# Kernel optimization log

Measured on AMD Instinct MI355X. Metric: run time of the kernel, lower is better.

## Reference

```python
import jax, jax.numpy as jnp
import numpy as np
from jax import lax

CLS_TOKEN_ID = 1


def _group_cumsum(x, reset_mask):
    # x: [B, S, D] float, reset_mask: [B, S] bool
    # Running sum that resets at the most recent position where reset_mask is True.
    s = jnp.cumsum(x, axis=1)                      # [B,S,D]
    prime = s - x                                  # exclusive cumsum [B,S,D]
    seq = jnp.arange(x.shape[1])                   # [S]
    idx = seq[None, :] * reset_mask.astype(jnp.int32)   # [B,S]
    idx = lax.cummax(idx, axis=1)[..., None]       # [B,S,1] index of last reset
    return s - jnp.take_along_axis(prime, idx, axis=1)


def group_cummean_weighted(embeddings, reset_mask):
    x = embeddings.astype(jnp.float32)
    ones = jnp.ones(reset_mask.shape + (1,), dtype=jnp.float32)  # [B,S,1]
    scale = _group_cumsum(ones, reset_mask)        # position-in-group count [B,S,1]
    out = _group_cumsum(x * scale, reset_mask) / scale
    return out.astype(embeddings.dtype)


def setup_inputs() -> dict:
    key = jax.random.key(0)
    k1, k2 = jax.random.split(key)
    B, S, D = 8, 4096, 1024
    embeddings = jax.random.normal(k1, (B, S, D), dtype=jnp.float32)
    input_ids = jax.random.randint(k2, (B, S), 0, 64, dtype=jnp.int64)
    return {"embeddings": embeddings, "input_ids": input_ids, "return_final": 0}


def reference(embeddings, input_ids, return_final):
    reset_mask = input_ids == CLS_TOKEN_ID         # [B,S] bool
    out = group_cummean_weighted(embeddings, reset_mask)
    if return_final:
        seq = jnp.arange(input_ids.shape[1])
        end_idx = jnp.max(jnp.where(reset_mask, seq, -1), axis=-1)  # [B]
        return out[jnp.arange(input_ids.shape[0]), end_idx]
    return out
```

## Files before the change

kernel.cpp:

```cpp
#include <hip/hip_runtime.h>


#define B_   8
#define S_   4096
#define D_   1024
#define CL   128
#define NCH  (S_/CL)
#define ROWS (B_*D_)

__global__ __launch_bounds__(256) void k0_count(const int* __restrict__ ids,
                                                float* __restrict__ cntf,
                                                float* __restrict__ invf) {
    int b = blockIdx.x;
    int t = threadIdx.x;
    const int PER = S_ / 256;
    __shared__ int lastr[256];

    int base = t * PER;
    const int* p = ids + b * S_ + base;
    int loc = -1;
#pragma unroll
    for (int j = 0; j < PER; j++)
        if (p[j] == 1) loc = base + j;
    lastr[t] = loc;
    __syncthreads();

    int g = 0;
    for (int i = 0; i < t; i++) {
        int v = lastr[i];
        g = v > g ? v : g;
    }
    for (int j = 0; j < PER; j++) {
        int s = base + j;
        if (p[j] == 1) g = s;
        float c = (float)(s - g + 1);
        cntf[b * S_ + s] = c;
        invf[b * S_ + s] = 1.0f / c;
    }
}

__global__ __launch_bounds__(256) void k1_partial(const float* __restrict__ X,
                                                  const float* __restrict__ cntf,
                                                  float* __restrict__ alpha,
                                                  float* __restrict__ gamma) {
    int blk = blockIdx.x;
    int dt  = blk & 3;
    int k   = (blk >> 2) & (NCH - 1);
    int b   = blk >> 7;
    int t   = threadIdx.x;

    __shared__ float cL[CL];
    if (t < CL) cL[t] = cntf[b * S_ + k * CL + t];
    __syncthreads();

    int d = dt * 256 + t;
    const float* p = X + (size_t)(b * S_ + k * CL) * D_ + d;

    float a = 0.f, g = 0.f;
#pragma unroll 8
    for (int j = 0; j < CL; j++) {
        float x  = p[(size_t)j * D_];
        float cf = cL[j];
        float wl = (float)(j + 1);
        float w  = cf < wl ? cf : wl;
        bool  rst = (cf == 1.0f);
        bool  pre = (cf > wl);
        a = fmaf(x, w, rst ? 0.f : a);
        g = rst ? 0.f : (pre ? g + x : g);
    }
    int row = b * D_ + d;
    alpha[k * ROWS + row] = a;
    gamma[k * ROWS + row] = g;
}

__global__ __launch_bounds__(256) void k2_scan(const float* __restrict__ alpha,
                                               const float* __restrict__ gamma,
                                               const float* __restrict__ cntf,
                                               float* __restrict__ Win) {
    int row = blockIdx.x * 256 + threadIdx.x;
    int b   = row >> 10;
    float W = 0.f, cin = 0.f;
    for (int k = 0; k < NCH; k++) {
        Win[k * ROWS + row] = W;
        float cend = cntf[b * S_ + (k + 1) * CL - 1];
        float a = alpha[k * ROWS + row];
        float g = gamma[k * ROWS + row];
        bool  has = (cend <= (float)CL);
        W   = has ? a : (a + W + g * cin);
        cin = cend;
    }
}

__global__ __launch_bounds__(256) void k3_out(const float* __restrict__ X,
                                              const float* __restrict__ cntf,
                                              const float* __restrict__ invf,
                                              const float* __restrict__ Win,
                                              float* __restrict__ out) {
    int blk = blockIdx.x;
    int dt  = blk & 3;
    int k   = (blk >> 2) & (NCH - 1);
    int b   = blk >> 7;
    int t   = threadIdx.x;

    __shared__ float cL[CL], iL[CL];
    if (t < CL) {
        cL[t] = cntf[b * S_ + k * CL + t];
        iL[t] = invf[b * S_ + k * CL + t];
    }
    __syncthreads();

    int d = dt * 256 + t;
    size_t off = (size_t)(b * S_ + k * CL) * D_ + d;
    const float* p = X + off;
    float*       q = out + off;

    float W = Win[k * ROWS + b * D_ + d];
#pragma unroll 8
    for (int j = 0; j < CL; j++) {
        float x  = p[(size_t)j * D_];
        float cf = cL[j];
        W = fmaf(x, cf, (cf == 1.0f) ? 0.f : W);
        q[(size_t)j * D_] = W * iL[j];
    }
}

extern "C" void kernel_launch(void* const* d_in, const int* in_sizes, int n_in,
                              void* d_out, int out_size, void* d_ws, size_t ws_size,
                              hipStream_t stream) {
    const float* X   = (const float*)d_in[0];
    const int*   ids = (const int*)d_in[1];
    float* out = (float*)d_out;

    float* cntf  = (float*)d_ws;
    float* invf  = cntf + B_ * S_;
    float* alpha = invf + B_ * S_;
    float* gamma = alpha + NCH * ROWS;
    float* Win   = gamma + NCH * ROWS;

    hipLaunchKernelGGL(k0_count,   dim3(B_),           dim3(256), 0, stream, ids, cntf, invf);
    hipLaunchKernelGGL(k1_partial, dim3(B_ * NCH * 4), dim3(256), 0, stream, X, cntf, alpha, gamma);
    hipLaunchKernelGGL(k2_scan,    dim3(ROWS / 256),   dim3(256), 0, stream, alpha, gamma, cntf, Win);
    hipLaunchKernelGGL(k3_out,     dim3(B_ * NCH * 4), dim3(256), 0, stream, X, cntf, invf, Win, out);
}
```

Baseline: 85.79 us.

## Vectorize chunked scan kernels to float4 and shrink chunk length

k1, k2 and k3 now work on float4 columns, so each thread handles four features with 128-bit loads and stores. The chunk length drops from 128 to 32 so the grid keeps enough blocks, and k3 writes its output with nontemporal stores to avoid polluting the cache. In exchange, the serial cross-chunk scan in k2 now runs 128 steps per row on only 8 blocks. The alpha, gamma and Win workspace buffers also grow four-fold, adding extra memory traffic and needing more workspace.

```diff
diff --git a/kernel.cpp b/kernel.cpp
--- a/kernel.cpp
+++ b/kernel.cpp
@@ -1,12 +1,15 @@
 #include <hip/hip_runtime.h>
 
 
-#define B_   8
-#define S_   4096
-#define D_   1024
-#define CL   128
-#define NCH  (S_/CL)
-#define ROWS (B_*D_)
+#define B_    8
+#define S_    4096
+#define D_    1024
+#define D4    (D_/4)
+#define CL    32
+#define NCH   (S_/CL)
+#define ROWS4 (B_*D4)
+
+typedef float f4 __attribute__((ext_vector_type(4)));
 
 __global__ __launch_bounds__(256) void k0_count(const int* __restrict__ ids,
                                                 float* __restrict__ cntf,
@@ -39,13 +42,12 @@
     }
 }
 
-__global__ __launch_bounds__(256) void k1_partial(const float* __restrict__ X,
+__global__ __launch_bounds__(256) void k1_partial(const f4* __restrict__ X,
                                                   const float* __restrict__ cntf,
-                                                  float* __restrict__ alpha,
-                                                  float* __restrict__ gamma) {
+                                                  f4* __restrict__ alpha,
+                                                  f4* __restrict__ gamma) {
     int blk = blockIdx.x;
-    int dt  = blk & 3;
-    int k   = (blk >> 2) & (NCH - 1);
+    int k   = blk & (NCH - 1);
     int b   = blk >> 7;
     int t   = threadIdx.x;
 
@@ -53,52 +55,50 @@
     if (t < CL) cL[t] = cntf[b * S_ + k * CL + t];
     __syncthreads();
 
-    int d = dt * 256 + t;
-    const float* p = X + (size_t)(b * S_ + k * CL) * D_ + d;
+    const f4* p = X + (size_t)(b * S_ + k * CL) * D4 + t;
 
-    float a = 0.f, g = 0.f;
+    f4 a = (f4)0.f, g = (f4)0.f;
 #pragma unroll 8
     for (int j = 0; j < CL; j++) {
-        float x  = p[(size_t)j * D_];
+        f4    x  = p[(size_t)j * D4];
         float cf = cL[j];
         float wl = (float)(j + 1);
         float w  = cf < wl ? cf : wl;
-        bool  rst = (cf == 1.0f);
-        bool  pre = (cf > wl);
-        a = fmaf(x, w, rst ? 0.f : a);
-        g = rst ? 0.f : (pre ? g + x : g);
+        if (cf == 1.0f) { a = (f4)0.f; g = (f4)0.f; }
+        a += x * w;
+        if (cf > wl) g += x;
     }
-    int row = b * D_ + d;
-    alpha[k * ROWS + row] = a;
-    gamma[k * ROWS + row] = g;
+    size_t r = (size_t)k * ROWS4 + b * D4 + t;
+    alpha[r] = a;
+    gamma[r] = g;
 }
 
-__global__ __launch_bounds__(256) void k2_scan(const float* __restrict__ alpha,
-                                               const float* __restrict__ gamma,
+__global__ __launch_bounds__(256) void k2_scan(const f4* __restrict__ alpha,
+                                               const f4* __restrict__ gamma,
                                                const float* __restrict__ cntf,
-                                               float* __restrict__ Win) {
-    int row = blockIdx.x * 256 + threadIdx.x;
-    int b   = row >> 10;
-    float W = 0.f, cin = 0.f;
+                                               f4* __restrict__ Win) {
+    int r = blockIdx.x * 256 + threadIdx.x;
+    int b = r >> 8;
+    f4 W = (f4)0.f;
+    float cin = 0.f;
     for (int k = 0; k < NCH; k++) {
-        Win[k * ROWS + row] = W;
+        Win[(size_t)k * ROWS4 + r] = W;
         float cend = cntf[b * S_ + (k + 1) * CL - 1];
-        float a = alpha[k * ROWS + row];
-        float g = gamma[k * ROWS + row];
-        bool  has = (cend <= (float)CL);
-        W   = has ? a : (a + W + g * cin);
+        f4 a = alpha[(size_t)k * ROWS4 + r];
+        f4 g = gamma[(size_t)k * ROWS4 + r];
+        if (cend <= (float)CL) W = a;
+        else                   W = a + W + g * cin;
         cin = cend;
     }
 }
 
-__global__ __launch_bounds__(256) void k3_out(const float* __restrict__ X,
+__global__ __launch_bounds__(256) void k3_out(const f4* __restrict__ X,
                                               const float* __restrict__ cntf,
                                               const float* __restrict__ invf,
-                                              const float* __restrict__ Win,
-                                              float* __restrict__ out) {
+                                              const f4* __restrict__ Win,
+                                              f4* __restrict__ out) {
     int blk = blockIdx.x;
-    int dt  = blk & 3;
-    int k   = (blk >> 2) & (NCH - 1);
+    int k   = blk & (NCH - 1);
     int b   = blk >> 7;
     int t   = threadIdx.x;
 
@@ -109,36 +109,36 @@
     }
     __syncthreads();
 
-    int d = dt * 256 + t;
-    size_t off = (size_t)(b * S_ + k * CL) * D_ + d;
-    const float* p = X + off;
-    float*       q = out + off;
+    size_t off = (size_t)(b * S_ + k * CL) * D4 + t;
+    const f4* p = X + off;
+    f4*       q = out + off;
 
-    float W = Win[k * ROWS + b * D_ + d];
+    f4 W = Win[(size_t)k * ROWS4 + b * D4 + t];
 #pragma unroll 8
     for (int j = 0; j < CL; j++) {
-        float x  = p[(size_t)j * D_];
+        f4    x  = p[(size_t)j * D4];
         float cf = cL[j];
-        W = fmaf(x, cf, (cf == 1.0f) ? 0.f : W);
-        q[(size_t)j * D_] = W * iL[j];
+        if (cf == 1.0f) W = (f4)0.f;
+        W += x * cf;
+        __builtin_nontemporal_store(W * iL[j], q + (size_t)j * D4);
     }
 }
 
 extern "C" void kernel_launch(void* const* d_in, const int* in_sizes, int n_in,
                               void* d_out, int out_size, void* d_ws, size_t ws_size,
                               hipStream_t stream) {
-    const float* X   = (const float*)d_in[0];
-    const int*   ids = (const int*)d_in[1];
-    float* out = (float*)d_out;
+    const f4*  X   = (const f4*)d_in[0];
+    const int* ids = (const int*)d_in[1];
+    f4* out = (f4*)d_out;
 
     float* cntf  = (float*)d_ws;
     float* invf  = cntf + B_ * S_;
-    float* alpha = invf + B_ * S_;
-    float* gamma = alpha + NCH * ROWS;
-    float* Win   = gamma + NCH * ROWS;
+    f4*    alpha = (f4*)(invf + B_ * S_);
+    f4*    gamma = alpha + (size_t)NCH * ROWS4;
+    f4*    Win   = gamma + (size_t)NCH * ROWS4;
 
-    hipLaunchKernelGGL(k0_count,   dim3(B_),           dim3(256), 0, stream, ids, cntf, invf);
-    hipLaunchKernelGGL(k1_partial, dim3(B_ * NCH * 4), dim3(256), 0, stream, X, cntf, alpha, gamma);
-    hipLaunchKernelGGL(k2_scan,    dim3(ROWS / 256),   dim3(256), 0, stream, alpha, gamma, cntf, Win);
-    hipLaunchKernelGGL(k3_out,     dim3(B_ * NCH * 4), dim3(256), 0, stream, X, cntf, invf, Win, out);
+    hipLaunchKernelGGL(k0_count,   dim3(B_),         dim3(256), 0, stream, ids, cntf, invf);
+    hipLaunchKernelGGL(k1_partial, dim3(B_ * NCH),   dim3(256), 0, stream, X, cntf, alpha, gamma);
+    hipLaunchKernelGGL(k2_scan,    dim3(ROWS4/256),  dim3(256), 0, stream, alpha, gamma, cntf, Win);
+    hipLaunchKernelGGL(k3_out,     dim3(B_ * NCH),   dim3(256), 0, stream, X, cntf, invf, Win, out);
 }
```

Result: slower. 126.9 us (+47.9%).
